# Kernel tuning notes

Measured on AMD Instinct MI355X. Metric: run time of the kernel, lower is better.

The kernel has to match this reference:

```python
import jax, jax.numpy as jnp
import numpy as np

T, K_FR, K_D, A = 2000, 400, 400, 100
EPS = 1e-24


def setup_inputs() -> dict:
    key = jax.random.key(0)
    ks = jax.random.split(key, 5)
    t = jnp.arange(T, dtype=jnp.float32)                      # uniform grid, dt = 1
    mask_spikes_fr = jax.random.randint(ks[0], (T, K_FR), 0, 2, dtype=jnp.int32)
    X_fr = jax.random.normal(ks[1], (T, K_FR, A), dtype=jnp.float32)
    theta = jax.random.normal(ks[2], (A,), dtype=jnp.float32) * 0.01  # keep r = exp(u) ~ O(1)
    phi_d = jax.random.normal(ks[3], (K_D,), dtype=jnp.float32)
    phi_fr = jax.random.normal(ks[4], (K_FR,), dtype=jnp.float32)
    return {"t": t, "mask_spikes_fr": mask_spikes_fr, "X_fr": X_fr,
            "theta": theta, "phi_d": phi_d, "phi_fr": phi_fr}


def _forward(t, mask_spikes_fr, X_fr, theta, phi_d, phi_fr, lam_mmd=1.0):
    dt = t[1] - t[0]
    m = mask_spikes_fr.astype(X_fr.dtype)                     # [T, K_fr] spike indicator
    u = jnp.einsum('tka,a->tk', X_fr, theta)                  # membrane potential
    r = jnp.exp(u)                                            # non_linearity = 'exp'
    # per-trial point-process log-likelihood: [K_fr]
    ll = jnp.sum(jnp.log(1.0 - jnp.exp(-dt * r) + EPS) * m - dt * r * (1.0 - m), axis=0)
    # score-function gradient of log-likelihood w.r.t. theta (r detached): [K_fr, A]
    r_d = jax.lax.stop_gradient(r)
    exp_r = jnp.exp(r_d * dt)
    g_ll = dt * jnp.einsum('tka,tk->ka', X_fr, r_d / (exp_r - 1.0 - EPS) * m) \
         - dt * jnp.einsum('tka,tk->ka', X_fr, r_d * (1.0 - m))
    # gramians from per-trial features phi
    g_ff = phi_fr[:, None] * phi_fr[None, :]                  # [K_fr, K_fr], symmetric
    g_df = phi_d[:, None] * phi_fr[None, :]                   # [K_d, K_fr]
    g_dd = phi_d[:, None] * phi_d[None, :]                    # [K_d, K_d], symmetric
    K_fr = phi_fr.shape[0]
    K_d = phi_d.shape[0]
    n_fr = K_fr * (K_fr - 1) // 2                             # number of triu (k=1) pairs
    n_d = K_d * (K_d - 1) // 2
    row_ff = jnp.sum(g_ff, axis=1)
    diag_ff = jnp.diagonal(g_ff)
    # mean over i<j of (ll_i + ll_j) * g_ff[i,j]; g_ff symmetric => (full - diag)/2
    mmd_grad = (jnp.dot(ll, row_ff) - jnp.dot(ll, diag_ff)) / n_fr \
             - 2.0 * jnp.mean(ll[None, :] * g_df)
    # mean over i<j of (g_ll_i + g_ll_j) * g_ff[i,j] per component a, minus cross term
    grad_theta = (jnp.einsum('ij,ia->a', g_ff, g_ll) - jnp.einsum('i,ia->a', diag_ff, g_ll)) / n_fr \
               - 2.0 * jnp.einsum('df,fa->a', g_df, g_ll) / (K_d * K_fr)
    # unbiased MMD: off-diagonal means of gramians
    tri_ff = (jnp.sum(g_ff) - jnp.sum(diag_ff)) / 2.0 / n_fr
    tri_dd = (jnp.sum(g_dd) - jnp.sum(jnp.diagonal(g_dd))) / 2.0 / n_d
    mmd = tri_dd + tri_ff - 2.0 * jnp.mean(g_df)
    return lam_mmd * mmd_grad, lam_mmd * grad_theta, mmd


def reference(t, mask_spikes_fr, X_fr, theta, phi_d, phi_fr):
    return _forward(t, mask_spikes_fr, X_fr, theta, phi_d, phi_fr)
```

## Files before the change

kernel.cpp:

```cpp
#include <hip/hip_runtime.h>

#define T_LEN   2000
#define K_FR    400
#define K_D     400
#define A_DIM   100
#define N_ROWS  (T_LEN * K_FR)
#define RPB     64
#define TILE_F  (RPB * A_DIM)
#define TILE_V4 (TILE_F / 4)
#define NBATCH  (N_ROWS / RPB)
#define EPSF    1e-24f
#define MAIN_BLOCKS 1024


__global__ void mmdglm_setup(const float* __restrict__ phi_d,
                             const float* __restrict__ phi_fr,
                             float* __restrict__ c,
                             float* __restrict__ gth_acc,
                             double* __restrict__ mmdg_acc,
                             float* __restrict__ out)
{
    __shared__ float w1[8], w2[8], w3[8], w4[8];
    __shared__ float sums[4];
    const int tid = threadIdx.x;
    const float vfr = (tid < K_FR) ? phi_fr[tid] : 0.f;
    const float vd  = (tid < K_D)  ? phi_d[tid]  : 0.f;
    float s1 = vfr, s2 = vfr * vfr, s3 = vd, s4 = vd * vd;
    #pragma unroll
    for (int off = 1; off < 64; off <<= 1) {
        s1 += __shfl_xor(s1, off);
        s2 += __shfl_xor(s2, off);
        s3 += __shfl_xor(s3, off);
        s4 += __shfl_xor(s4, off);
    }
    const int wave = tid >> 6, lane = tid & 63;
    if (lane == 0) { w1[wave] = s1; w2[wave] = s2; w3[wave] = s3; w4[wave] = s4; }
    __syncthreads();
    if (tid == 0) {
        float a = 0, b = 0, cc = 0, d = 0;
        for (int i = 0; i < 8; ++i) { a += w1[i]; b += w2[i]; cc += w3[i]; d += w4[i]; }
        sums[0] = a; sums[1] = b; sums[2] = cc; sums[3] = d;
    }
    __syncthreads();
    const float S_fr = sums[0], Q_fr = sums[1], S_d = sums[2], Q_d = sums[3];
    const float n_fr = (float)(K_FR * (K_FR - 1) / 2);
    const float n_d  = (float)(K_D * (K_D - 1) / 2);
    if (tid < K_FR) {
        const float p = phi_fr[tid];
        c[tid] = (S_fr * p - p * p) / n_fr
               - 2.0f * S_d * p / (float)(K_D * K_FR);
    }
    if (tid < A_DIM) gth_acc[tid] = 0.f;
    if (tid == 511) *mmdg_acc = 0.0;
    if (tid == 0) {
        const float mmd = (S_d * S_d - Q_d) / (2.0f * n_d)
                        + (S_fr * S_fr - Q_fr) / (2.0f * n_fr)
                        - 2.0f * S_d * S_fr / (float)(K_D * K_FR);
        out[101] = mmd;
    }
}

__global__ __launch_bounds__(256)
void mmdglm_main(const float* __restrict__ X,
                 const int*   __restrict__ mask,
                 const float* __restrict__ theta,
                 const float* __restrict__ tvec,
                 const float* __restrict__ c,
                 float*  __restrict__ gth_acc,
                 double* __restrict__ mmdg_acc)
{
    __shared__ __align__(16) float tile[TILE_F];
    __shared__ float lred[4];
    const int tid  = threadIdx.x;
    const int slot = tid >> 2;
    const int part = tid & 3;

    float th[25];
    #pragma unroll
    for (int j = 0; j < 25; ++j) th[j] = theta[part * 25 + j];

    const float dt = tvec[1] - tvec[0];

    float acc[25];
    #pragma unroll
    for (int j = 0; j < 25; ++j) acc[j] = 0.f;
    float llacc = 0.f;

    for (int b = blockIdx.x; b < NBATCH; b += gridDim.x) {
        const int row0 = b * RPB;
        const float4* src = (const float4*)(X + (size_t)row0 * A_DIM);
        for (int i = tid; i < TILE_V4; i += 256)
            ((float4*)tile)[i] = src[i];
        __syncthreads();

        const int row = row0 + slot;
        const float* xp = tile + 25 * tid;
        float x[25];
        float u = 0.f;
        #pragma unroll
        for (int j = 0; j < 25; ++j) { x[j] = xp[j]; u = fmaf(x[j], th[j], u); }
        u += __shfl_xor(u, 1);
        u += __shfl_xor(u, 2);

        const float r  = __expf(u);
        const int   m  = mask[row];
        const float ck = c[row - (row / K_FR) * K_FR];
        float w, llt;
        if (m) {
            const float eneg = __expf(-dt * r);
            const float epos = __expf(dt * r);
            llt = __logf(1.0f - eneg + EPSF);
            w   = dt * r / (epos - 1.0f - EPSF);
        } else {
            llt = -dt * r;
            w   = -dt * r;
        }
        const float cw = ck * w;
        if (part == 0) llacc = fmaf(ck, llt, llacc);
        #pragma unroll
        for (int j = 0; j < 25; ++j) acc[j] = fmaf(cw, x[j], acc[j]);
        __syncthreads();
    }

    #pragma unroll
    for (int j = 0; j < 25; ++j) tile[tid * 25 + j] = acc[j];
    __syncthreads();
    if (tid < A_DIM) {
        const int p = tid / 25, j = tid - p * 25;
        float s = 0.f;
        for (int sl = 0; sl < RPB; ++sl)
            s += tile[(sl * 4 + p) * 25 + j];
        atomicAdd(&gth_acc[tid], s);
    }

    float l = llacc;
    #pragma unroll
    for (int off = 1; off < 64; off <<= 1) l += __shfl_xor(l, off);
    const int wave = tid >> 6, lane = tid & 63;
    if (lane == 0) lred[wave] = l;
    __syncthreads();
    if (tid == 0)
        atomicAdd(mmdg_acc, (double)(lred[0] + lred[1] + lred[2] + lred[3]));
}

__global__ void mmdglm_finalize(const double* __restrict__ mmdg_acc,
                                const float* __restrict__ gth_acc,
                                float* __restrict__ out)
{
    const int tid = threadIdx.x;
    if (tid == 0) out[0] = (float)(*mmdg_acc);
    if (tid >= 1 && tid <= 100) out[tid] = gth_acc[tid - 1];
}

extern "C" void kernel_launch(void* const* d_in, const int* in_sizes, int n_in,
                              void* d_out, int out_size, void* d_ws, size_t ws_size,
                              hipStream_t stream) {
    const float* t      = (const float*)d_in[0];
    const int*   mask   = (const int*)  d_in[1];
    const float* X      = (const float*)d_in[2];
    const float* theta  = (const float*)d_in[3];
    const float* phi_d  = (const float*)d_in[4];
    const float* phi_fr = (const float*)d_in[5];
    float* out = (float*)d_out;

    char* ws = (char*)d_ws;
    double* mmdg_acc = (double*)ws;
    float*  gth_acc  = (float*)(ws + 8);
    float*  c        = (float*)(ws + 416);

    mmdglm_setup<<<1, 512, 0, stream>>>(phi_d, phi_fr, c, gth_acc, mmdg_acc, out);
    mmdglm_main<<<MAIN_BLOCKS, 256, 0, stream>>>(X, mask, theta, t, c, gth_acc, mmdg_acc);
    mmdglm_finalize<<<1, 128, 0, stream>>>(mmdg_acc, gth_acc, out);
}
```

Measured before the change: 461.9 us.

## Load X directly from global with interleaved columns, drop LDS tile staging

Each thread now reads its 25 elements of a row straight from global memory with stride 4, so the four threads of a row together cover contiguous addresses. Theta is indexed to match this interleaving. The shared-memory tile copy and both per-iteration barriers are gone, and the final per-block reduction uses wave shuffles followed by a small LDS stage. The grid also grows to 1280 blocks. The intent is to remove the LDS round trip and the synchronisation stalls from this memory-bound stream. The cost is that global loads become scalar dword loads instead of float4, with a strided per-lane pattern whose coalescing depends on the hardware.

```diff
diff --git a/kernel.cpp b/kernel.cpp
--- a/kernel.cpp
+++ b/kernel.cpp
@@ -6,11 +6,9 @@
 #define A_DIM   100
 #define N_ROWS  (T_LEN * K_FR)
 #define RPB     64
-#define TILE_F  (RPB * A_DIM)
-#define TILE_V4 (TILE_F / 4)
 #define NBATCH  (N_ROWS / RPB)
 #define EPSF    1e-24f
-#define MAIN_BLOCKS 1024
+#define MAIN_BLOCKS 1280
 
 
 __global__ void mmdglm_setup(const float* __restrict__ phi_d,
@@ -69,7 +67,7 @@
                  float*  __restrict__ gth_acc,
                  double* __restrict__ mmdg_acc)
 {
-    __shared__ __align__(16) float tile[TILE_F];
+    __shared__ float red[4 * A_DIM];
     __shared__ float lred[4];
     const int tid  = threadIdx.x;
     const int slot = tid >> 2;
@@ -77,7 +75,7 @@
 
     float th[25];
     #pragma unroll
-    for (int j = 0; j < 25; ++j) th[j] = theta[part * 25 + j];
+    for (int j = 0; j < 25; ++j) th[j] = theta[part + 4 * j];
 
     const float dt = tvec[1] - tvec[0];
 
@@ -87,58 +85,57 @@
     float llacc = 0.f;
 
     for (int b = blockIdx.x; b < NBATCH; b += gridDim.x) {
-        const int row0 = b * RPB;
-        const float4* src = (const float4*)(X + (size_t)row0 * A_DIM);
-        for (int i = tid; i < TILE_V4; i += 256)
-            ((float4*)tile)[i] = src[i];
-        __syncthreads();
+        const int row = b * RPB + slot;
+        const float* xp = X + (size_t)row * A_DIM + part;
 
-        const int row = row0 + slot;
-        const float* xp = tile + 25 * tid;
         float x[25];
         float u = 0.f;
         #pragma unroll
-        for (int j = 0; j < 25; ++j) { x[j] = xp[j]; u = fmaf(x[j], th[j], u); }
+        for (int j = 0; j < 25; ++j) { x[j] = xp[4 * j]; u = fmaf(x[j], th[j], u); }
         u += __shfl_xor(u, 1);
         u += __shfl_xor(u, 2);
 
         const float r  = __expf(u);
         const int   m  = mask[row];
-        const float ck = c[row - (row / K_FR) * K_FR];
+        const float ck = c[row % K_FR];
         float w, llt;
         if (m) {
-            const float eneg = __expf(-dt * r);
-            const float epos = __expf(dt * r);
-            llt = __logf(1.0f - eneg + EPSF);
-            w   = dt * r / (epos - 1.0f - EPSF);
+            const float dr = dt * r;
+            llt = __logf(1.0f - __expf(-dr) + EPSF);
+            w   = dr / (__expf(dr) - 1.0f - EPSF);
         } else {
-            llt = -dt * r;
             w   = -dt * r;
+            llt = w;
         }
         const float cw = ck * w;
         if (part == 0) llacc = fmaf(ck, llt, llacc);
         #pragma unroll
         for (int j = 0; j < 25; ++j) acc[j] = fmaf(cw, x[j], acc[j]);
-        __syncthreads();
     }
 
     #pragma unroll
-    for (int j = 0; j < 25; ++j) tile[tid * 25 + j] = acc[j];
-    __syncthreads();
-    if (tid < A_DIM) {
-        const int p = tid / 25, j = tid - p * 25;
-        float s = 0.f;
-        for (int sl = 0; sl < RPB; ++sl)
-            s += tile[(sl * 4 + p) * 25 + j];
-        atomicAdd(&gth_acc[tid], s);
+    for (int j = 0; j < 25; ++j) {
+        acc[j] += __shfl_xor(acc[j], 4);
+        acc[j] += __shfl_xor(acc[j], 8);
+        acc[j] += __shfl_xor(acc[j], 16);
+        acc[j] += __shfl_xor(acc[j], 32);
+    }
+    const int wave = tid >> 6, lane = tid & 63;
+    if (lane < 4) {
+        #pragma unroll
+        for (int j = 0; j < 25; ++j)
+            red[wave * A_DIM + lane + 4 * j] = acc[j];
     }
 
     float l = llacc;
     #pragma unroll
     for (int off = 1; off < 64; off <<= 1) l += __shfl_xor(l, off);
-    const int wave = tid >> 6, lane = tid & 63;
     if (lane == 0) lred[wave] = l;
     __syncthreads();
+
+    if (tid < A_DIM)
+        atomicAdd(&gth_acc[tid],
+                  red[tid] + red[A_DIM + tid] + red[2 * A_DIM + tid] + red[3 * A_DIM + tid]);
     if (tid == 0)
         atomicAdd(mmdg_acc, (double)(lred[0] + lred[1] + lred[2] + lred[3]));
 }
```

Result: no change. 470.6 us (+1.9%).
